# Kernel tuning notes

Measured on AMD Instinct MI355X. Metric: run time of the kernel, lower is better.

The kernel has to match this reference:

```python
import jax, jax.numpy as jnp
import numpy as np

NPOINT = 1024
RADIUS = 0.2
NSAMPLE = 32
MLP = (64, 64, 128)
EPS = 1e-5  # torch BatchNorm2d default


def farthest_point_sample(xyz, npoint):
    """xyz: [B,N,3] -> centroid indices [B,npoint] (deterministic start at index 0)."""
    B, N, _ = xyz.shape

    def step(carry, _):
        distance, farthest = carry  # [B,N], [B]
        centroid = jnp.take_along_axis(xyz, farthest[:, None, None], axis=1)  # [B,1,3]
        dist = jnp.sum((xyz - centroid) ** 2, axis=-1)  # [B,N]
        distance = jnp.minimum(distance, dist)
        new_farthest = jnp.argmax(distance, axis=-1)
        return (distance, new_farthest), farthest

    init = (jnp.full((B, N), 1e10, xyz.dtype), jnp.zeros((B,), jnp.int32))
    _, centroids = jax.lax.scan(step, init, None, length=npoint)  # [npoint,B]
    return centroids.T  # [B,npoint]


def ball_query(xyz, new_xyz, radius, nsample):
    """xyz:[B,N,3], new_xyz:[B,M,3] -> group_idx [B,M,nsample]."""
    N = xyz.shape[1]
    # sqrdists[b,m,n] = ||new_xyz[b,m] - xyz[b,n]||^2
    sqrdists = jnp.sum((new_xyz[:, :, None, :] - xyz[:, None, :, :]) ** 2, axis=-1)  # [B,M,N]
    idx = jnp.where(sqrdists > radius * radius, N, jnp.arange(N, dtype=jnp.int32))
    idx = jnp.sort(idx, axis=-1)[:, :, :nsample]
    return jnp.where(idx == N, 0, idx)  # out-of-ball slots fall back to point 0 (as in source)


def index_points(points, idx):
    """points:[B,N,C], idx:[B,M,K] -> [B,M,K,C]."""
    B, M, K = idx.shape
    flat = idx.reshape(B, M * K)
    out = jnp.take_along_axis(points, flat[:, :, None], axis=1)
    return out.reshape(B, M, K, points.shape[-1])


def _forward(xyz, points, layers):
    B = xyz.shape[0]
    fps_idx = farthest_point_sample(xyz, NPOINT)
    new_xyz = jnp.take_along_axis(xyz, fps_idx[:, :, None], axis=1)  # [B,M,3]
    group_idx = ball_query(xyz, new_xyz, RADIUS, NSAMPLE)  # [B,M,K]
    grouped_xyz = index_points(xyz, group_idx) - new_xyz[:, :, None, :]  # [B,M,K,3]
    x = jnp.concatenate([grouped_xyz, index_points(points, group_idx)], axis=-1)  # [B,M,K,3+C]
    # shared MLP: 1x1 conv + BatchNorm (training-mode batch stats) + ReLU
    for (w, b, g, be) in layers:
        x = jnp.einsum('bmkc,oc->bmko', x, w) + b
        mean = jnp.mean(x, axis=(0, 1, 2))
        var = jnp.var(x, axis=(0, 1, 2))  # biased, matches torch BN normalization
        x = jax.nn.relu(g * (x - mean) * jax.lax.rsqrt(var + EPS) + be)
    new_points = jnp.max(x, axis=2)  # [B,M,Cout]
    return new_xyz, new_points


def setup_inputs() -> dict:
    key = jax.random.key(0)
    ks = jax.random.split(key, 2 + len(MLP))
    B, N, C = 16, 4096, 64
    inp = {
        'xyz': jax.random.uniform(ks[0], (B, N, 3), jnp.float32),
        'points': jax.random.normal(ks[1], (B, N, C), jnp.float32),
    }
    last = 3 + C
    for i, out_ch in enumerate(MLP):
        inp[f'w{i}'] = jax.random.normal(ks[2 + i], (out_ch, last), jnp.float32) / np.sqrt(last).astype(np.float32)
        inp[f'b{i}'] = jnp.zeros((out_ch,), jnp.float32)
        inp[f'g{i}'] = jnp.ones((out_ch,), jnp.float32)
        inp[f'be{i}'] = jnp.zeros((out_ch,), jnp.float32)
        last = out_ch
    return inp


def reference(xyz, points, w0, b0, g0, be0, w1, b1, g1, be1, w2, b2, g2, be2):
    layers = [(w0, b0, g0, be0), (w1, b1, g1, be1), (w2, b2, g2, be2)]
    return _forward(xyz, points, layers)
```

## Files before the change

kernel.cpp:

```cpp
#include <hip/hip_runtime.h>

typedef unsigned int uint;
typedef unsigned short ushort;
typedef unsigned long long u64;

#define N_PTS 4096
#define B_SZ 16
#define M_PTS 1024
#define K_SMP 32
#define NROWS (B_SZ*M_PTS*K_SMP)
#define INV_CNT (1.0f/524288.0f)

__device__ __forceinline__ float sqdist3(float ax,float ay,float az,float bx,float by,float bz){
  float dx=__fsub_rn(ax,bx), dy=__fsub_rn(ay,by), dz=__fsub_rn(az,bz);
  return __fadd_rn(__fadd_rn(__fmul_rn(dx,dx),__fmul_rn(dy,dy)),__fmul_rn(dz,dz));
}
__device__ __forceinline__ ushort f2bf(float x){
  uint u = __float_as_uint(x);
  u = (u + 0x7fffu + ((u>>16)&1u)) >> 16;
  return (ushort)u;
}
__device__ __forceinline__ float bf2f(uint u){ return __uint_as_float(u<<16); }

__device__ __forceinline__ void kmerge(uint& kl, uint& kh, uint okl, uint okh){
  u64 a = ((u64)kh << 32) | kl;
  u64 b = ((u64)okh << 32) | okl;
  bool t = b > a;
  kl = t ? okl : kl;
  kh = t ? okh : kh;
}
template<int CTRL>
__device__ __forceinline__ uint dppu(uint v){
  return (uint)__builtin_amdgcn_update_dpp((int)v, (int)v, CTRL, 0xf, 0xf, false);
}
template<int CTRL>
__device__ __forceinline__ void dppkmerge(uint& kl, uint& kh){
  uint okl = dppu<CTRL>(kl);
  uint okh = dppu<CTRL>(kh);
  kmerge(kl, kh, okl, okh);
}

__global__ __launch_bounds__(512, 2) void fps_kernel(const float* __restrict__ xyz,
                                                     float* __restrict__ out_newxyz){
  const int b = blockIdx.x;
  const int t = threadIdx.x;
  __shared__ float4 sxyz[N_PTS];
  __shared__ uint   xch[2][8][2];
  const float* src = xyz + (size_t)b*N_PTS*3;
  float px[8], py[8], pz[8], dist[8];
  uint nl[8];
#pragma unroll
  for (int i=0;i<8;i++){
    const int p = t + 512*i;
    float x = src[3*p+0], y = src[3*p+1], z = src[3*p+2];
    px[i]=x; py[i]=y; pz[i]=z;
    dist[i]=1e10f; nl[i] = ~(uint)p;
    sxyz[p] = make_float4(x, y, z, 0.f);
  }
  __syncthreads();
  float cx, cy, cz;
  { float4 c0 = sxyz[0]; cx=c0.x; cy=c0.y; cz=c0.z; }
  const int w = t >> 6, lane = t & 63;
  float* outx = out_newxyz + (size_t)b*M_PTS*3;
  for (int s = 0; s < M_PTS; ++s){
    if (t == 0){ outx[s*3+0]=cx; outx[s*3+1]=cy; outx[s*3+2]=cz; }
    uint khv[8];
#pragma unroll
    for (int i=0;i<8;i++){
      float d  = sqdist3(px[i],py[i],pz[i],cx,cy,cz);
      float nd = fminf(dist[i], d);
      dist[i] = nd;
      khv[i] = __float_as_uint(nd);
    }
    uint l0=nl[0], h0=khv[0]; kmerge(l0,h0,nl[1],khv[1]);
    uint l1=nl[2], h1=khv[2]; kmerge(l1,h1,nl[3],khv[3]);
    uint l2=nl[4], h2=khv[4]; kmerge(l2,h2,nl[5],khv[5]);
    uint l3=nl[6], h3=khv[6]; kmerge(l3,h3,nl[7],khv[7]);
    kmerge(l0,h0,l1,h1); kmerge(l2,h2,l3,h3); kmerge(l0,h0,l2,h2);
    uint al=l0, ah=h0;
    dppkmerge<0x111>(al, ah);
    dppkmerge<0x112>(al, ah);
    dppkmerge<0x114>(al, ah);
    dppkmerge<0x118>(al, ah);
    dppkmerge<0x142>(al, ah);
    dppkmerge<0x143>(al, ah);
    const int par = s & 1;
    if (lane == 63){ xch[par][w][0] = al; xch[par][w][1] = ah; }
    __syncthreads();
    uint ckl = xch[par][lane & 7][0];
    uint ckh = xch[par][lane & 7][1];
    dppkmerge<0x111>(ckl, ckh);
    dppkmerge<0x112>(ckl, ckh);
    dppkmerge<0x114>(ckl, ckh);
    uint wkl = (uint)__builtin_amdgcn_readlane((int)ckl, 7);
    uint idx = ~wkl;
    float4 cc = sxyz[idx];
    cx = cc.x; cy = cc.y; cz = cc.z;
  }
}

__global__ __launch_bounds__(256) void ballq_kernel(const float* __restrict__ xyz,
                                                    const float* __restrict__ newxyz,
                                                    int* __restrict__ gidx){
  const int blk = blockIdx.x;
  const int b = blk >> 6;
  const int mbase = (blk & 63) * 16;
  __shared__ float sx[N_PTS], sy[N_PTS], sz[N_PTS];
  const float* src = xyz + (size_t)b*N_PTS*3;
  for (int i = threadIdx.x; i < N_PTS*3; i += 256){
    float v = src[i]; int p = i/3, j = i%3;
    (j==0?sx:(j==1?sy:sz))[p] = v;
  }
  __syncthreads();
  const int w = threadIdx.x >> 6, lane = threadIdx.x & 63;
  const float R2 = (float)(0.2*0.2);
  for (int mm = w; mm < 16; mm += 4){
    const int m = mbase + mm;
    const float* c = newxyz + ((size_t)b*M_PTS + m)*3;
    float cx = c[0], cy = c[1], cz = c[2];
    int* gout = gidx + ((size_t)b*M_PTS + m)*K_SMP;
    int cnt = 0;
    for (int base = 0; base < N_PTS && cnt < K_SMP; base += 64){
      int p = base + lane;
      float d = sqdist3(sx[p],sy[p],sz[p],cx,cy,cz);
      bool in = (d <= R2);
      unsigned long long mask = __ballot(in);
      int prefix = __popcll(mask & ((1ull << lane) - 1ull));
      int slot = cnt + prefix;
      if (in && slot < K_SMP) gout[slot] = p;
      cnt += __popcll(mask);
    }
    if (cnt < K_SMP){
      int slot = cnt + lane;
      if (slot < K_SMP) gout[slot] = 0;
    }
  }
}

__global__ __launch_bounds__(256) void conv0_kernel(const float* __restrict__ xyz,
                                                    const float* __restrict__ points,
                                                    const float* __restrict__ newxyz,
                                                    const int* __restrict__ gidx,
                                                    const float* __restrict__ W0,
                                                    const float* __restrict__ b0,
                                                    ushort* __restrict__ x1){
  __shared__ float A [67][68];
  __shared__ float Bw[67][68];
  __shared__ float sb[64];
  const int tid = threadIdx.x;
  if (tid < 64) sb[tid] = b0[tid];
  for (int idx = tid; idx < 64*67; idx += 256){
    int o = idx / 67, k = idx - o*67;
    Bw[k][o] = W0[idx];
  }
  const size_t rbase = (size_t)blockIdx.x * 64;
  {
    const int r = tid & 63;
    const int q = tid >> 6;
    const int R = (int)rbase + r;
    const int b_ = R >> 15, m_ = (R >> 5) & 1023;
    const int g_ = gidx[R];
    const float4* p4 = (const float4*)(points + (((size_t)(b_<<12) + g_) << 6) + q*16);
#pragma unroll
    for (int j=0;j<4;j++){
      float4 v = p4[j];
      int c = 3 + q*16 + j*4;
      A[c+0][r]=v.x; A[c+1][r]=v.y; A[c+2][r]=v.z; A[c+3][r]=v.w;
    }
    if (q == 0){
      const float* pc = newxyz + ((size_t)(b_<<10) + m_)*3;
      const float* pp = xyz    + ((size_t)(b_<<12) + g_)*3;
      A[0][r] = pp[0]-pc[0];
      A[1][r] = pp[1]-pc[1];
      A[2][r] = pp[2]-pc[2];
    }
  }
  __syncthreads();
  const int tr = tid >> 4, tc = tid & 15;
  float acc[4][4];
#pragma unroll
  for (int i=0;i<4;i++)
#pragma unroll
    for (int j=0;j<4;j++) acc[i][j] = sb[tc*4+j];
#pragma unroll 4
  for (int k=0;k<67;k++){
    float4 a = *(const float4*)&A [k][tr*4];
    float4 w = *(const float4*)&Bw[k][tc*4];
    acc[0][0]=fmaf(a.x,w.x,acc[0][0]); acc[0][1]=fmaf(a.x,w.y,acc[0][1]);
    acc[0][2]=fmaf(a.x,w.z,acc[0][2]); acc[0][3]=fmaf(a.x,w.w,acc[0][3]);
    acc[1][0]=fmaf(a.y,w.x,acc[1][0]); acc[1][1]=fmaf(a.y,w.y,acc[1][1]);
    acc[1][2]=fmaf(a.y,w.z,acc[1][2]); acc[1][3]=fmaf(a.y,w.w,acc[1][3]);
    acc[2][0]=fmaf(a.z,w.x,acc[2][0]); acc[2][1]=fmaf(a.z,w.y,acc[2][1]);
    acc[2][2]=fmaf(a.z,w.z,acc[2][2]); acc[2][3]=fmaf(a.z,w.w,acc[2][3]);
    acc[3][0]=fmaf(a.w,w.x,acc[3][0]); acc[3][1]=fmaf(a.w,w.y,acc[3][1]);
    acc[3][2]=fmaf(a.w,w.z,acc[3][2]); acc[3][3]=fmaf(a.w,w.w,acc[3][3]);
  }
#pragma unroll
  for (int i=0;i<4;i++){
    uint2 v;
    v.x = (uint)f2bf(acc[i][0]) | ((uint)f2bf(acc[i][1])<<16);
    v.y = (uint)f2bf(acc[i][2]) | ((uint)f2bf(acc[i][3])<<16);
    *(uint2*)(x1 + ((rbase + tr*4 + i) << 6) + tc*4) = v;
  }
}

template<int OSTRIDE>
__global__ __launch_bounds__(256) void convg_kernel(const ushort* __restrict__ xin,
                                                    const float* __restrict__ Sv,
                                                    const float* __restrict__ SSv,
                                                    const float* __restrict__ gg,
                                                    const float* __restrict__ be,
                                                    const float* __restrict__ W,
                                                    const float* __restrict__ bias,
                                                    ushort* __restrict__ xout){
  __shared__ float A [64][68];
  __shared__ float Bw[64][68];
  __shared__ float sc[64], sh[64], sb[64];
  const int tid = threadIdx.x;
  const int ocol0 = blockIdx.y * 64;
  if (tid < 64){
    int c = tid;
    float mean = Sv[c]*INV_CNT;
    float var  = fmaf(-mean, mean, SSv[c]*INV_CNT);
    float is   = rsqrtf(var + 1e-5f);
    float scv  = gg[c]*is;
    sc[c] = scv; sh[c] = fmaf(-mean, scv, be[c]);
    sb[c] = bias[ocol0 + c];
  }
  {
    const int o  = tid & 63;
    const int kq = tid >> 6;
    const float* wrow = W + (size_t)(ocol0 + o)*64;
#pragma unroll
    for (int kk=0;kk<4;kk++){
      int k = (kq + 4*kk)*4;
      float4 wv = *(const float4*)(wrow + k);
      Bw[k+0][o]=wv.x; Bw[k+1][o]=wv.y; Bw[k+2][o]=wv.z; Bw[k+3][o]=wv.w;
    }
  }
  __syncthreads();
  const size_t rbase = (size_t)blockIdx.x * 64;
  {
    const int r   = tid & 63;
    const int kg0 = tid >> 6;
#pragma unroll
    for (int kk=0;kk<2;kk++){
      const int kg = kg0 + 4*kk;
      uint4 v = *(const uint4*)(xin + ((rbase + r) << 6) + kg*8);
      uint d[4] = {v.x,v.y,v.z,v.w};
#pragma unroll
      for (int q=0;q<4;q++){
        int k = kg*8 + 2*q;
        float a0 = bf2f(d[q] & 0xffffu), a1 = bf2f(d[q] >> 16);
        A[k+0][r] = fmaxf(fmaf(a0, sc[k+0], sh[k+0]), 0.f);
        A[k+1][r] = fmaxf(fmaf(a1, sc[k+1], sh[k+1]), 0.f);
      }
    }
  }
  __syncthreads();
  const int tr = tid >> 4, tc = tid & 15;
  float acc[4][4];
#pragma unroll
  for (int i=0;i<4;i++)
#pragma unroll
    for (int j=0;j<4;j++) acc[i][j] = sb[tc*4+j];
#pragma unroll 4
  for (int k=0;k<64;k++){
    float4 a = *(const float4*)&A [k][tr*4];
    float4 w = *(const float4*)&Bw[k][tc*4];
    acc[0][0]=fmaf(a.x,w.x,acc[0][0]); acc[0][1]=fmaf(a.x,w.y,acc[0][1]);
    acc[0][2]=fmaf(a.x,w.z,acc[0][2]); acc[0][3]=fmaf(a.x,w.w,acc[0][3]);
    acc[1][0]=fmaf(a.y,w.x,acc[1][0]); acc[1][1]=fmaf(a.y,w.y,acc[1][1]);
    acc[1][2]=fmaf(a.y,w.z,acc[1][2]); acc[1][3]=fmaf(a.y,w.w,acc[1][3]);
    acc[2][0]=fmaf(a.z,w.x,acc[2][0]); acc[2][1]=fmaf(a.z,w.y,acc[2][1]);
    acc[2][2]=fmaf(a.z,w.z,acc[2][2]); acc[2][3]=fmaf(a.z,w.w,acc[2][3]);
    acc[3][0]=fmaf(a.w,w.x,acc[3][0]); acc[3][1]=fmaf(a.w,w.y,acc[3][1]);
    acc[3][2]=fmaf(a.w,w.z,acc[3][2]); acc[3][3]=fmaf(a.w,w.w,acc[3][3]);
  }
#pragma unroll
  for (int i=0;i<4;i++){
    uint2 v;
    v.x = (uint)f2bf(acc[i][0]) | ((uint)f2bf(acc[i][1])<<16);
    v.y = (uint)f2bf(acc[i][2]) | ((uint)f2bf(acc[i][3])<<16);
    *(uint2*)(xout + (rbase + tr*4 + i)*OSTRIDE + ocol0 + tc*4) = v;
  }
}

template<int C>
__global__ __launch_bounds__(256) void stats_kernel(const ushort* __restrict__ x,
                                                    float* __restrict__ S,
                                                    float* __restrict__ SS){
  constexpr int GRP = C/8;
  constexpr int RL  = 256/GRP;
  const int cg = threadIdx.x % GRP;
  const int rl = threadIdx.x / GRP;
  const int rows_per_block = NROWS / 1024;
  const int r0 = blockIdx.x * rows_per_block;
  float s[8], ss[8];
#pragma unroll
  for (int j=0;j<8;j++){ s[j]=0.f; ss[j]=0.f; }
  for (int r = r0 + rl; r < r0 + rows_per_block; r += RL){
    uint4 v = *(const uint4*)(x + (size_t)r*C + cg*8);
    uint d[4] = {v.x, v.y, v.z, v.w};
#pragma unroll
    for (int q=0;q<4;q++){
      float a0 = bf2f(d[q] & 0xffffu), a1 = bf2f(d[q] >> 16);
      s[2*q]   += a0; ss[2*q]   = fmaf(a0, a0, ss[2*q]);
      s[2*q+1] += a1; ss[2*q+1] = fmaf(a1, a1, ss[2*q+1]);
    }
  }
  __shared__ float ls[256][8], lss[256][8];
#pragma unroll
  for (int j=0;j<8;j++){ ls[threadIdx.x][j]=s[j]; lss[threadIdx.x][j]=ss[j]; }
  __syncthreads();
  if (threadIdx.x < C){
    const int grp = threadIdx.x >> 3, j = threadIdx.x & 7;
    float a = 0.f, q2 = 0.f;
#pragma unroll
    for (int q = 0; q < RL; q++){ a += ls[q*GRP + grp][j]; q2 += lss[q*GRP + grp][j]; }
    atomicAdd(&S[threadIdx.x], a); atomicAdd(&SS[threadIdx.x], q2);
  }
}

__global__ __launch_bounds__(256) void maxpool_kernel(const ushort* __restrict__ x3,
                                                      const float* __restrict__ S2,
                                                      const float* __restrict__ SS2,
                                                      const float* __restrict__ g2,
                                                      const float* __restrict__ be2,
                                                      float* __restrict__ outp){
  const int lane = threadIdx.x & 63, wv = threadIdx.x >> 6;
  const int bm = blockIdx.x*4 + wv;
  const int c0 = lane*2, c1 = c0+1;
  float mean0 = S2[c0]*INV_CNT;
  float var0  = fmaf(-mean0, mean0, SS2[c0]*INV_CNT);
  float s0 = g2[c0]*rsqrtf(var0+1e-5f);
  float h0 = fmaf(-mean0, s0, be2[c0]);
  float mean1 = S2[c1]*INV_CNT;
  float var1  = fmaf(-mean1, mean1, SS2[c1]*INV_CNT);
  float s1 = g2[c1]*rsqrtf(var1+1e-5f);
  float h1 = fmaf(-mean1, s1, be2[c1]);
  const uint* rb = (const uint*)(x3 + (size_t)bm*K_SMP*128);
  float mx0 = 0.f, mx1 = 0.f;
#pragma unroll
  for (int k=0;k<K_SMP;k++){
    uint v = rb[k*64 + lane];
    float a0 = bf2f(v & 0xffffu), a1 = bf2f(v >> 16);
    mx0 = fmaxf(mx0, fmaxf(fmaf(a0, s0, h0), 0.f));
    mx1 = fmaxf(mx1, fmaxf(fmaf(a1, s1, h1), 0.f));
  }
  float2* o2 = (float2*)(outp + (size_t)bm*128);
  o2[lane] = make_float2(mx0, mx1);
}

extern "C" void kernel_launch(void* const* d_in, const int* in_sizes, int n_in,
                              void* d_out, int out_size, void* d_ws, size_t ws_size,
                              hipStream_t stream){
  const float* xyz    = (const float*)d_in[0];
  const float* points = (const float*)d_in[1];
  const float* w0  = (const float*)d_in[2];
  const float* b0  = (const float*)d_in[3];
  const float* g0  = (const float*)d_in[4];
  const float* be0 = (const float*)d_in[5];
  const float* w1  = (const float*)d_in[6];
  const float* b1  = (const float*)d_in[7];
  const float* g1  = (const float*)d_in[8];
  const float* be1 = (const float*)d_in[9];
  const float* w2  = (const float*)d_in[10];
  const float* b2  = (const float*)d_in[11];
  const float* g2  = (const float*)d_in[12];
  const float* be2 = (const float*)d_in[13];

  float* out      = (float*)d_out;
  float* newxyz   = out;
  float* outp     = out + (size_t)B_SZ*M_PTS*3;

  char* ws = (char*)d_ws;
  int*   gidx  = (int*)ws;
  float* stats = (float*)(ws + (2u<<20));
  float* S0 = stats,      *SS0 = stats+64;
  float* S1 = stats+128,  *SS1 = stats+192;
  float* S2 = stats+256,  *SS2 = stats+384;
  ushort* x1 = (ushort*)(ws + (4u<<20));
  ushort* x3 = (ushort*)(ws + (4u<<20));
  ushort* x2 = (ushort*)(ws + (4u<<20) + 134217728u);

  hipMemsetAsync(stats, 0, 512*sizeof(float), stream);
  fps_kernel  <<<B_SZ, 512, 0, stream>>>(xyz, newxyz);
  ballq_kernel<<<1024, 256, 0, stream>>>(xyz, newxyz, gidx);
  conv0_kernel<<<NROWS/64, 256, 0, stream>>>(xyz, points, newxyz, gidx, w0, b0, x1);
  stats_kernel<64><<<1024, 256, 0, stream>>>(x1, S0, SS0);
  convg_kernel<64><<<dim3(NROWS/64, 1), 256, 0, stream>>>(x1, S0, SS0, g0, be0, w1, b1, x2);
  stats_kernel<64><<<1024, 256, 0, stream>>>(x2, S1, SS1);
  convg_kernel<128><<<dim3(NROWS/64, 2), 256, 0, stream>>>(x2, S1, SS1, g1, be1, w2, b2, x3);
  stats_kernel<128><<<1024, 256, 0, stream>>>(x3, S2, SS2);
  maxpool_kernel<<<NROWS/128, 256, 0, stream>>>(x3, S2, SS2, g2, be2, outp);
}
```

Before: 1.122 ms.

## Enlarge conv GEMM tiles to 128 rows with 8xN register blocking per thread

The three pointwise-conv GEMM kernels now process 128 rows per block, and each thread holds an 8x4 or 8x8 accumulator tile instead of 4x4. The layer-2 kernel computes all 128 output channels in one block instead of splitting them across two grid-y blocks, so the input tile is loaded and normalized once. This raises FMA-per-LDS-load intensity and removes duplicated input staging. In exchange it uses more registers and LDS per block, which can reduce occupancy, and launch_bounds(256,2) limits register allocation.

```diff
diff --git a/kernel.cpp b/kernel.cpp
--- a/kernel.cpp
+++ b/kernel.cpp
@@ -137,14 +137,14 @@
   }
 }
 
-__global__ __launch_bounds__(256) void conv0_kernel(const float* __restrict__ xyz,
-                                                    const float* __restrict__ points,
-                                                    const float* __restrict__ newxyz,
-                                                    const int* __restrict__ gidx,
-                                                    const float* __restrict__ W0,
-                                                    const float* __restrict__ b0,
-                                                    ushort* __restrict__ x1){
-  __shared__ float A [67][68];
+__global__ __launch_bounds__(256, 2) void conv0_kernel(const float* __restrict__ xyz,
+                                                       const float* __restrict__ points,
+                                                       const float* __restrict__ newxyz,
+                                                       const int* __restrict__ gidx,
+                                                       const float* __restrict__ W0,
+                                                       const float* __restrict__ b0,
+                                                       ushort* __restrict__ x1){
+  __shared__ float A [67][132];
   __shared__ float Bw[67][68];
   __shared__ float sb[64];
   const int tid = threadIdx.x;
@@ -153,21 +153,21 @@
     int o = idx / 67, k = idx - o*67;
     Bw[k][o] = W0[idx];
   }
-  const size_t rbase = (size_t)blockIdx.x * 64;
+  const size_t rbase = (size_t)blockIdx.x * 128;
   {
-    const int r = tid & 63;
-    const int q = tid >> 6;
+    const int r  = tid & 127;
+    const int hf = tid >> 7;
     const int R = (int)rbase + r;
     const int b_ = R >> 15, m_ = (R >> 5) & 1023;
     const int g_ = gidx[R];
-    const float4* p4 = (const float4*)(points + (((size_t)(b_<<12) + g_) << 6) + q*16);
-#pragma unroll
-    for (int j=0;j<4;j++){
+    const float4* p4 = (const float4*)(points + (((size_t)(b_<<12) + g_) << 6) + hf*32);
+#pragma unroll
+    for (int j=0;j<8;j++){
       float4 v = p4[j];
-      int c = 3 + q*16 + j*4;
+      int c = 3 + hf*32 + j*4;
       A[c+0][r]=v.x; A[c+1][r]=v.y; A[c+2][r]=v.z; A[c+3][r]=v.w;
     }
-    if (q == 0){
+    if (hf == 0){
       const float* pc = newxyz + ((size_t)(b_<<10) + m_)*3;
       const float* pp = xyz    + ((size_t)(b_<<12) + g_)*3;
       A[0][r] = pp[0]-pc[0];
@@ -177,47 +177,46 @@
   }
   __syncthreads();
   const int tr = tid >> 4, tc = tid & 15;
-  float acc[4][4];
-#pragma unroll
-  for (int i=0;i<4;i++)
+  float acc[8][4];
+#pragma unroll
+  for (int i=0;i<8;i++)
 #pragma unroll
     for (int j=0;j<4;j++) acc[i][j] = sb[tc*4+j];
 #pragma unroll 4
   for (int k=0;k<67;k++){
-    float4 a = *(const float4*)&A [k][tr*4];
-    float4 w = *(const float4*)&Bw[k][tc*4];
-    acc[0][0]=fmaf(a.x,w.x,acc[0][0]); acc[0][1]=fmaf(a.x,w.y,acc[0][1]);
-    acc[0][2]=fmaf(a.x,w.z,acc[0][2]); acc[0][3]=fmaf(a.x,w.w,acc[0][3]);
-    acc[1][0]=fmaf(a.y,w.x,acc[1][0]); acc[1][1]=fmaf(a.y,w.y,acc[1][1]);
-    acc[1][2]=fmaf(a.y,w.z,acc[1][2]); acc[1][3]=fmaf(a.y,w.w,acc[1][3]);
-    acc[2][0]=fmaf(a.z,w.x,acc[2][0]); acc[2][1]=fmaf(a.z,w.y,acc[2][1]);
-    acc[2][2]=fmaf(a.z,w.z,acc[2][2]); acc[2][3]=fmaf(a.z,w.w,acc[2][3]);
-    acc[3][0]=fmaf(a.w,w.x,acc[3][0]); acc[3][1]=fmaf(a.w,w.y,acc[3][1]);
-    acc[3][2]=fmaf(a.w,w.z,acc[3][2]); acc[3][3]=fmaf(a.w,w.w,acc[3][3]);
-  }
-#pragma unroll
-  for (int i=0;i<4;i++){
+    float4 a0 = *(const float4*)&A [k][tr*8];
+    float4 a1 = *(const float4*)&A [k][tr*8+4];
+    float4 w  = *(const float4*)&Bw[k][tc*4];
+    float av[8] = {a0.x,a0.y,a0.z,a0.w,a1.x,a1.y,a1.z,a1.w};
+#pragma unroll
+    for (int i=0;i<8;i++){
+      acc[i][0]=fmaf(av[i],w.x,acc[i][0]);
+      acc[i][1]=fmaf(av[i],w.y,acc[i][1]);
+      acc[i][2]=fmaf(av[i],w.z,acc[i][2]);
+      acc[i][3]=fmaf(av[i],w.w,acc[i][3]);
+    }
+  }
+#pragma unroll
+  for (int i=0;i<8;i++){
     uint2 v;
     v.x = (uint)f2bf(acc[i][0]) | ((uint)f2bf(acc[i][1])<<16);
     v.y = (uint)f2bf(acc[i][2]) | ((uint)f2bf(acc[i][3])<<16);
-    *(uint2*)(x1 + ((rbase + tr*4 + i) << 6) + tc*4) = v;
-  }
-}
-
-template<int OSTRIDE>
-__global__ __launch_bounds__(256) void convg_kernel(const ushort* __restrict__ xin,
-                                                    const float* __restrict__ Sv,
-                                                    const float* __restrict__ SSv,
-                                                    const float* __restrict__ gg,
-                                                    const float* __restrict__ be,
-                                                    const float* __restrict__ W,
-                                                    const float* __restrict__ bias,
-                                                    ushort* __restrict__ xout){
-  __shared__ float A [64][68];
+    *(uint2*)(x1 + ((rbase + tr*8 + i) << 6) + tc*4) = v;
+  }
+}
+
+__global__ __launch_bounds__(256, 2) void convg64_kernel(const ushort* __restrict__ xin,
+                                                         const float* __restrict__ Sv,
+                                                         const float* __restrict__ SSv,
+                                                         const float* __restrict__ gg,
+                                                         const float* __restrict__ be,
+                                                         const float* __restrict__ W,
+                                                         const float* __restrict__ bias,
+                                                         ushort* __restrict__ xout){
+  __shared__ float A [64][132];
   __shared__ float Bw[64][68];
   __shared__ float sc[64], sh[64], sb[64];
   const int tid = threadIdx.x;
-  const int ocol0 = blockIdx.y * 64;
   if (tid < 64){
     int c = tid;
     float mean = Sv[c]*INV_CNT;
@@ -225,32 +224,32 @@
     float is   = rsqrtf(var + 1e-5f);
     float scv  = gg[c]*is;
     sc[c] = scv; sh[c] = fmaf(-mean, scv, be[c]);
-    sb[c] = bias[ocol0 + c];
+    sb[c] = bias[c];
   }
   {
     const int o  = tid & 63;
     const int kq = tid >> 6;
-    const float* wrow = W + (size_t)(ocol0 + o)*64;
-#pragma unroll
-    for (int kk=0;kk<4;kk++){
-      int k = (kq + 4*kk)*4;
-      float4 wv = *(const float4*)(wrow + k);
+    const float* wrow = W + (size_t)o*64 + kq*16;
+#pragma unroll
+    for (int q=0;q<4;q++){
+      float4 wv = *(const float4*)(wrow + q*4);
+      int k = kq*16 + q*4;
       Bw[k+0][o]=wv.x; Bw[k+1][o]=wv.y; Bw[k+2][o]=wv.z; Bw[k+3][o]=wv.w;
     }
   }
   __syncthreads();
-  const size_t rbase = (size_t)blockIdx.x * 64;
+  const size_t rbase = (size_t)blockIdx.x * 128;
   {
-    const int r   = tid & 63;
-    const int kg0 = tid >> 6;
-#pragma unroll
-    for (int kk=0;kk<2;kk++){
-      const int kg = kg0 + 4*kk;
-      uint4 v = *(const uint4*)(xin + ((rbase + r) << 6) + kg*8);
+    const int r  = tid & 127;
+    const int kh = tid >> 7;
+    const uint4* src = (const uint4*)(xin + ((rbase + r) << 6) + kh*32);
+#pragma unroll
+    for (int g=0; g<4; g++){
+      uint4 v = src[g];
       uint d[4] = {v.x,v.y,v.z,v.w};
 #pragma unroll
       for (int q=0;q<4;q++){
-        int k = kg*8 + 2*q;
+        int k = kh*32 + g*8 + 2*q;
         float a0 = bf2f(d[q] & 0xffffu), a1 = bf2f(d[q] >> 16);
         A[k+0][r] = fmaxf(fmaf(a0, sc[k+0], sh[k+0]), 0.f);
         A[k+1][r] = fmaxf(fmaf(a1, sc[k+1], sh[k+1]), 0.f);
@@ -259,30 +258,114 @@
   }
   __syncthreads();
   const int tr = tid >> 4, tc = tid & 15;
-  float acc[4][4];
-#pragma unroll
-  for (int i=0;i<4;i++)
+  float acc[8][4];
+#pragma unroll
+  for (int i=0;i<8;i++)
 #pragma unroll
     for (int j=0;j<4;j++) acc[i][j] = sb[tc*4+j];
 #pragma unroll 4
   for (int k=0;k<64;k++){
-    float4 a = *(const float4*)&A [k][tr*4];
-    float4 w = *(const float4*)&Bw[k][tc*4];
-    acc[0][0]=fmaf(a.x,w.x,acc[0][0]); acc[0][1]=fmaf(a.x,w.y,acc[0][1]);
-    acc[0][2]=fmaf(a.x,w.z,acc[0][2]); acc[0][3]=fmaf(a.x,w.w,acc[0][3]);
-    acc[1][0]=fmaf(a.y,w.x,acc[1][0]); acc[1][1]=fmaf(a.y,w.y,acc[1][1]);
-    acc[1][2]=fmaf(a.y,w.z,acc[1][2]); acc[1][3]=fmaf(a.y,w.w,acc[1][3]);
-    acc[2][0]=fmaf(a.z,w.x,acc[2][0]); acc[2][1]=fmaf(a.z,w.y,acc[2][1]);
-    acc[2][2]=fmaf(a.z,w.z,acc[2][2]); acc[2][3]=fmaf(a.z,w.w,acc[2][3]);
-    acc[3][0]=fmaf(a.w,w.x,acc[3][0]); acc[3][1]=fmaf(a.w,w.y,acc[3][1]);
-    acc[3][2]=fmaf(a.w,w.z,acc[3][2]); acc[3][3]=fmaf(a.w,w.w,acc[3][3]);
-  }
-#pragma unroll
-  for (int i=0;i<4;i++){
+    float4 a0 = *(const float4*)&A [k][tr*8];
+    float4 a1 = *(const float4*)&A [k][tr*8+4];
+    float4 w  = *(const float4*)&Bw[k][tc*4];
+    float av[8] = {a0.x,a0.y,a0.z,a0.w,a1.x,a1.y,a1.z,a1.w};
+#pragma unroll
+    for (int i=0;i<8;i++){
+      acc[i][0]=fmaf(av[i],w.x,acc[i][0]);
+      acc[i][1]=fmaf(av[i],w.y,acc[i][1]);
+      acc[i][2]=fmaf(av[i],w.z,acc[i][2]);
+      acc[i][3]=fmaf(av[i],w.w,acc[i][3]);
+    }
+  }
+#pragma unroll
+  for (int i=0;i<8;i++){
     uint2 v;
     v.x = (uint)f2bf(acc[i][0]) | ((uint)f2bf(acc[i][1])<<16);
     v.y = (uint)f2bf(acc[i][2]) | ((uint)f2bf(acc[i][3])<<16);
-    *(uint2*)(xout + (rbase + tr*4 + i)*OSTRIDE + ocol0 + tc*4) = v;
+    *(uint2*)(xout + ((rbase + tr*8 + i) << 6) + tc*4) = v;
+  }
+}
+
+__global__ __launch_bounds__(256, 2) void convg128_kernel(const ushort* __restrict__ xin,
+                                                          const float* __restrict__ Sv,
+                                                          const float* __restrict__ SSv,
+                                                          const float* __restrict__ gg,
+                                                          const float* __restrict__ be,
+                                                          const float* __restrict__ W,
+                                                          const float* __restrict__ bias,
+                                                          ushort* __restrict__ xout){
+  __shared__ float A [64][132];
+  __shared__ float Bw[64][132];
+  __shared__ float sc[64], sh[64], sb[128];
+  const int tid = threadIdx.x;
+  if (tid < 64){
+    int c = tid;
+    float mean = Sv[c]*INV_CNT;
+    float var  = fmaf(-mean, mean, SSv[c]*INV_CNT);
+    float is   = rsqrtf(var + 1e-5f);
+    float scv  = gg[c]*is;
+    sc[c] = scv; sh[c] = fmaf(-mean, scv, be[c]);
+  }
+  if (tid < 128) sb[tid] = bias[tid];
+  {
+    const int o  = tid & 127;
+    const int kh = tid >> 7;
+    const float* wrow = W + (size_t)o*64 + kh*32;
+#pragma unroll
+    for (int q=0;q<8;q++){
+      float4 wv = *(const float4*)(wrow + q*4);
+      int k = kh*32 + q*4;
+      Bw[k+0][o]=wv.x; Bw[k+1][o]=wv.y; Bw[k+2][o]=wv.z; Bw[k+3][o]=wv.w;
+    }
+  }
+  __syncthreads();
+  const size_t rbase = (size_t)blockIdx.x * 128;
+  {
+    const int r  = tid & 127;
+    const int kh = tid >> 7;
+    const uint4* src = (const uint4*)(xin + ((rbase + r) << 6) + kh*32);
+#pragma unroll
+    for (int g=0; g<4; g++){
+      uint4 v = src[g];
+      uint d[4] = {v.x,v.y,v.z,v.w};
+#pragma unroll
+      for (int q=0;q<4;q++){
+        int k = kh*32 + g*8 + 2*q;
+        float a0 = bf2f(d[q] & 0xffffu), a1 = bf2f(d[q] >> 16);
+        A[k+0][r] = fmaxf(fmaf(a0, sc[k+0], sh[k+0]), 0.f);
+        A[k+1][r] = fmaxf(fmaf(a1, sc[k+1], sh[k+1]), 0.f);
+      }
+    }
+  }
+  __syncthreads();
+  const int tr = tid >> 4, tc = tid & 15;
+  float acc[8][8];
+#pragma unroll
+  for (int i=0;i<8;i++)
+#pragma unroll
+    for (int j=0;j<8;j++) acc[i][j] = sb[tc*8+j];
+#pragma unroll 2
+  for (int k=0;k<64;k++){
+    float4 a0 = *(const float4*)&A [k][tr*8];
+    float4 a1 = *(const float4*)&A [k][tr*8+4];
+    float4 w0 = *(const float4*)&Bw[k][tc*8];
+    float4 w1 = *(const float4*)&Bw[k][tc*8+4];
+    float av[8] = {a0.x,a0.y,a0.z,a0.w,a1.x,a1.y,a1.z,a1.w};
+    float wv[8] = {w0.x,w0.y,w0.z,w0.w,w1.x,w1.y,w1.z,w1.w};
+#pragma unroll
+    for (int i=0;i<8;i++)
+#pragma unroll
+      for (int j=0;j<8;j++)
+        acc[i][j] = fmaf(av[i], wv[j], acc[i][j]);
+  }
+#pragma unroll
+  for (int i=0;i<8;i++){
+    uint4 v;
+    v.x = (uint)f2bf(acc[i][0]) | ((uint)f2bf(acc[i][1])<<16);
+    v.y = (uint)f2bf(acc[i][2]) | ((uint)f2bf(acc[i][3])<<16);
+    v.z = (uint)f2bf(acc[i][4]) | ((uint)f2bf(acc[i][5])<<16);
+    v.w = (uint)f2bf(acc[i][6]) | ((uint)f2bf(acc[i][7])<<16);
+    *(uint4*)(xout + ((rbase + tr*8 + i) << 7) + tc*8) = v;
   }
 }
 
@@ -387,11 +470,11 @@
   hipMemsetAsync(stats, 0, 512*sizeof(float), stream);
   fps_kernel  <<<B_SZ, 512, 0, stream>>>(xyz, newxyz);
   ballq_kernel<<<1024, 256, 0, stream>>>(xyz, newxyz, gidx);
-  conv0_kernel<<<NROWS/64, 256, 0, stream>>>(xyz, points, newxyz, gidx, w0, b0, x1);
+  conv0_kernel<<<NROWS/128, 256, 0, stream>>>(xyz, points, newxyz, gidx, w0, b0, x1);
   stats_kernel<64><<<1024, 256, 0, stream>>>(x1, S0, SS0);
-  convg_kernel<64><<<dim3(NROWS/64, 1), 256, 0, stream>>>(x1, S0, SS0, g0, be0, w1, b1, x2);
+  convg64_kernel<<<NROWS/128, 256, 0, stream>>>(x1, S0, SS0, g0, be0, w1, b1, x2);
   stats_kernel<64><<<1024, 256, 0, stream>>>(x2, S1, SS1);
-  convg_kernel<128><<<dim3(NROWS/64, 2), 256, 0, stream>>>(x2, S1, SS1, g1, be1, w2, b2, x3);
+  convg128_kernel<<<NROWS/128, 256, 0, stream>>>(x2, S1, SS1, g1, be1, w2, b2, x3);
   stats_kernel<128><<<1024, 256, 0, stream>>>(x3, S2, SS2);
   maxpool_kernel<<<NROWS/128, 256, 0, stream>>>(x3, S2, SS2, g2, be2, outp);
 }
```

Result: no change. 1.102 ms (-1.7%).
